# Kernel optimization log

Hardware: AMD Instinct MI355X
Metric: run time of the kernel (lower is better)

The kernel has to match this reference:

```python
import jax, jax.numpy as jnp
import numpy as np

EPS = 1.0
POS_WEIGHT = 1.0
REDUCTION = 'mean'

N, D = 8192, 128
NUM_CLASSES = 32


def setup_inputs() -> dict:
    key = jax.random.key(0)
    k1, k2 = jax.random.split(key)
    ys = jax.random.normal(k1, (N, D), dtype=jnp.float32)
    labels = jax.random.randint(k2, (N,), 0, NUM_CLASSES, dtype=jnp.int64)
    return {"ys": ys, "labels": labels}


def reference(ys, labels):
    n = ys.shape[0]
    # Pairwise squared distances via one GEMM: ||a||^2 + ||b||^2 - 2 a.b
    sq = jnp.sum(ys * ys, axis=-1)                      # [N]
    d2 = sq[:, None] + sq[None, :] - 2.0 * (ys @ ys.T)  # [N, N]
    d2 = jnp.maximum(d2, 0.0)
    pair = jnp.triu(jnp.ones((n, n), dtype=bool), k=1)  # i < j, each unordered pair once
    same = labels[:, None] == labels[None, :]
    # positive-pair term: pos_weight * squared distance
    pos = POS_WEIGHT * d2
    # negative-pair term: clip(eps - sqrt(d2), 0)^2 ; guard sqrt(0) for unused entries
    neg_mask = pair & (~same)
    d = jnp.sqrt(jnp.where(neg_mask, d2, 1.0))
    neg = jnp.clip(EPS - d, 0.0) ** 2
    terms = jnp.where(same, pos, neg) * pair.astype(ys.dtype)
    loss = jnp.sum(terms)
    if REDUCTION == 'mean':
        loss = loss / (n * (n - 1) / 2)
    return loss.reshape(1)
```

## Files before the change

kernel.cpp:

```cpp
#include <hip/hip_runtime.h>
#include <hip/hip_bf16.h>
#include <stdint.h>
#include <math.h>

#define NN 8192
#define DD 128
#define NB 64
#define NBLK (NB * (NB + 1) / 2)

typedef __attribute__((ext_vector_type(8))) short short8;
typedef __attribute__((ext_vector_type(4))) float f32x4;

__device__ __forceinline__ unsigned short f2bf_rne(float x) {
    union { float f; uint32_t u; } v; v.f = x;
    uint32_t r = v.u + 0x7FFFu + ((v.u >> 16) & 1u);
    return (unsigned short)(r >> 16);
}

__global__ __launch_bounds__(256) void prep_kernel(const float* __restrict__ ys,
                                                   unsigned short* __restrict__ ybf,
                                                   float* __restrict__ sq) {
    int row = blockIdx.x * 8 + (threadIdx.x >> 5);
    int c = threadIdx.x & 31;
    float4 v = ((const float4*)(ys + (size_t)row * DD))[c];
    ushort4 o;
    o.x = f2bf_rne(v.x); o.y = f2bf_rne(v.y); o.z = f2bf_rne(v.z); o.w = f2bf_rne(v.w);
    ((ushort4*)(ybf + (size_t)row * DD))[c] = o;
    float s = v.x * v.x + v.y * v.y + v.z * v.z + v.w * v.w;
#pragma unroll
    for (int m = 16; m >= 1; m >>= 1) s += __shfl_xor(s, m);
    if (c == 0) sq[row] = s;
}

__global__ __launch_bounds__(256, 4) void loss_kernel(const unsigned short* __restrict__ ybf,
                                                      const float* __restrict__ sq,
                                                      const int* __restrict__ lab,
                                                      float* __restrict__ partial) {
    int p = blockIdx.x;
    int q = (NBLK - 1) - p;
    int r = (int)((sqrtf(8.0f * (float)q + 1.0f) - 1.0f) * 0.5f);
    while (r * (r + 1) / 2 > q) --r;
    while ((r + 1) * (r + 2) / 2 <= q) ++r;
    int bi = (NB - 1) - r;
    int bj = (NB - 1) - (q - r * (r + 1) / 2);

    __shared__ __align__(16) unsigned char smA[16384];
    __shared__ __align__(16) unsigned char smB[16384];
    __shared__ float sqA[128], sqB[128];
    __shared__ int labA[128], labB[128];
    __shared__ float wsum[4];

    int t = threadIdx.x;
    int i0 = bi * 128, j0 = bj * 128;

    if (t < 128) { sqA[t] = sq[i0 + t]; labA[t] = lab[i0 + t]; }
    else         { int u = t - 128; sqB[u] = sq[j0 + u]; labB[u] = lab[j0 + u]; }

    int wave = t >> 6, lane = t & 63;
    int wm = wave >> 1, wn = wave & 1;
    int lr = lane & 15, lg = lane >> 4;

    f32x4 acc[4][4];
#pragma unroll
    for (int m = 0; m < 4; ++m)
#pragma unroll
        for (int n = 0; n < 4; ++n) acc[m][n] = (f32x4){0.f, 0.f, 0.f, 0.f};

#pragma unroll
    for (int h = 0; h < 2; ++h) {
#pragma unroll
        for (int k = 0; k < 4; ++k) {
            int idx = k * 256 + t;
            int row = idx >> 3, c8 = idx & 7;
            uint4 va = *(const uint4*)(ybf + (size_t)(i0 + row) * DD + h * 64 + c8 * 8);
            uint4 vb = *(const uint4*)(ybf + (size_t)(j0 + row) * DD + h * 64 + c8 * 8);
            *(uint4*)(smA + row * 128 + ((c8 ^ (row & 7)) << 4)) = va;
            *(uint4*)(smB + row * 128 + ((c8 ^ (row & 7)) << 4)) = vb;
        }
        __syncthreads();
#pragma unroll
        for (int ks = 0; ks < 2; ++ks) {
            int c = ks * 4 + lg;
            short8 af[4], bfr[4];
#pragma unroll
            for (int m = 0; m < 4; ++m) {
                int row = wm * 64 + m * 16 + lr;
                af[m] = *(const short8*)(smA + row * 128 + ((c ^ (row & 7)) << 4));
            }
#pragma unroll
            for (int n = 0; n < 4; ++n) {
                int row = wn * 64 + n * 16 + lr;
                bfr[n] = *(const short8*)(smB + row * 128 + ((c ^ (row & 7)) << 4));
            }
#pragma unroll
            for (int m = 0; m < 4; ++m)
#pragma unroll
                for (int n = 0; n < 4; ++n)
                    acc[m][n] = __builtin_amdgcn_mfma_f32_16x16x32_bf16(af[m], bfr[n], acc[m][n], 0, 0, 0);
        }
        __syncthreads();
    }

    float lsum = 0.f;
#pragma unroll
    for (int n = 0; n < 4; ++n) {
        int jl = wn * 64 + n * 16 + lr;
        float sqj = sqB[jl];
        int lj = labB[jl];
        int j = j0 + jl;
#pragma unroll
        for (int m = 0; m < 4; ++m) {
#pragma unroll
            for (int q2 = 0; q2 < 4; ++q2) {
                int il = wm * 64 + m * 16 + lg * 4 + q2;
                int i = i0 + il;
                float d2 = fmaxf(sqA[il] + sqj - 2.0f * acc[m][n][q2], 0.0f);
                float term;
                if (labA[il] == lj) {
                    term = d2;
                } else if (d2 < 1.0f) {
                    float dd = 1.0f - sqrtf(d2);
                    term = dd * dd;
                } else {
                    term = 0.0f;
                }
                if (i < j) lsum += term;
            }
        }
    }

    lsum *= (2.0f / ((float)NN * (float)(NN - 1)));

#pragma unroll
    for (int off = 32; off >= 1; off >>= 1) lsum += __shfl_down(lsum, off);
    if (lane == 0) wsum[wave] = lsum;
    __syncthreads();
    if (t == 0) partial[p] = wsum[0] + wsum[1] + wsum[2] + wsum[3];
}

__global__ __launch_bounds__(256) void reduce_kernel(const float* __restrict__ partial,
                                                     float* __restrict__ out) {
    int t = threadIdx.x;
    float s = 0.f;
    for (int p = t; p < NBLK; p += 256) s += partial[p];
#pragma unroll
    for (int off = 32; off >= 1; off >>= 1) s += __shfl_down(s, off);
    __shared__ float ws[4];
    if ((t & 63) == 0) ws[t >> 6] = s;
    __syncthreads();
    if (t == 0) out[0] = ws[0] + ws[1] + ws[2] + ws[3];
}

extern "C" void kernel_launch(void* const* d_in, const int* in_sizes, int n_in,
                              void* d_out, int out_size, void* d_ws, size_t ws_size,
                              hipStream_t stream) {
    const float* ys = (const float*)d_in[0];
    const int* lab = (const int*)d_in[1];
    float* out = (float*)d_out;

    unsigned short* ybf = (unsigned short*)d_ws;
    float* sq = (float*)((char*)d_ws + (size_t)NN * DD * 2);
    float* partial = (float*)((char*)d_ws + (size_t)NN * DD * 2 + NN * 4);

    prep_kernel<<<NN / 8, 256, 0, stream>>>(ys, ybf, sq);
    loss_kernel<<<NBLK, 256, 0, stream>>>(ybf, sq, lab, partial);
    reduce_kernel<<<1, 256, 0, stream>>>(partial, out);
}
```

Baseline: 34.52 us.

## Compute positive-pair loss via class sums and skip far negative tiles

The positive-pair term now comes in closed form from per-class sums, counts and squared norms (n_c*sum||y||^2 - ||sum y||^2), so the tile loop handles only negative pairs. The ±2 scaling is folded into a negated, rounded bf16 copy of A, and the sq terms are preloaded into the accumulators, so the MFMA output is d2 directly. Operands are stored in an MFMA-fragment layout and read straight from global memory, with no LDS staging or barriers. Wavefronts whose tiles contain no d2 < 1 skip the negative epilogue entirely. In exchange it relies on random data rarely producing close pairs, adds float atomics (making summation order nondeterministic), and the bf16 rounding of the negated copy plus class-sum cancellation may shift accuracy.

```diff
diff --git a/kernel.cpp b/kernel.cpp
--- a/kernel.cpp
+++ b/kernel.cpp
@@ -7,6 +7,8 @@
 #define DD 128
 #define NB 64
 #define NBLK (NB * (NB + 1) / 2)
+#define NC 32
+#define NPB 32
 
 typedef __attribute__((ext_vector_type(8))) short short8;
 typedef __attribute__((ext_vector_type(4))) float f32x4;
@@ -17,138 +19,187 @@
     return (unsigned short)(r >> 16);
 }
 
+
 __global__ __launch_bounds__(256) void prep_kernel(const float* __restrict__ ys,
-                                                   unsigned short* __restrict__ ybf,
-                                                   float* __restrict__ sq) {
-    int row = blockIdx.x * 8 + (threadIdx.x >> 5);
-    int c = threadIdx.x & 31;
-    float4 v = ((const float4*)(ys + (size_t)row * DD))[c];
-    ushort4 o;
-    o.x = f2bf_rne(v.x); o.y = f2bf_rne(v.y); o.z = f2bf_rne(v.z); o.w = f2bf_rne(v.w);
-    ((ushort4*)(ybf + (size_t)row * DD))[c] = o;
-    float s = v.x * v.x + v.y * v.y + v.z * v.z + v.w * v.w;
-#pragma unroll
-    for (int m = 16; m >= 1; m >>= 1) s += __shfl_xor(s, m);
-    if (c == 0) sq[row] = s;
-}
-
-__global__ __launch_bounds__(256, 4) void loss_kernel(const unsigned short* __restrict__ ybf,
-                                                      const float* __restrict__ sq,
-                                                      const int* __restrict__ lab,
-                                                      float* __restrict__ partial) {
-    int p = blockIdx.x;
+                                                   const int* __restrict__ lab,
+                                                   unsigned short* __restrict__ ybfA,
+                                                   unsigned short* __restrict__ ybfB,
+                                                   float* __restrict__ sq,
+                                                   float* __restrict__ clspart,
+                                                   float* __restrict__ clscnt,
+                                                   float* __restrict__ clssq,
+                                                   float* __restrict__ negacc) {
+    int b = blockIdx.x, t = threadIdx.x;
+    __shared__ float cls[NC][DD];
+    __shared__ float cnt[NC], csq[NC];
+    if (b < 512) {
+        int row = b * 16 + (t >> 4), c8 = t & 15;
+        const float* base = ys + (size_t)row * DD + c8 * 8;
+        float4 v0 = *(const float4*)base;
+        float4 v1 = *(const float4*)(base + 4);
+        uint32_t w0 = (uint32_t)f2bf_rne(v0.x) | ((uint32_t)f2bf_rne(v0.y) << 16);
+        uint32_t w1 = (uint32_t)f2bf_rne(v0.z) | ((uint32_t)f2bf_rne(v0.w) << 16);
+        uint32_t w2 = (uint32_t)f2bf_rne(v1.x) | ((uint32_t)f2bf_rne(v1.y) << 16);
+        uint32_t w3 = (uint32_t)f2bf_rne(v1.z) | ((uint32_t)f2bf_rne(v1.w) << 16);
+        uint4 outB = make_uint4(w0, w1, w2, w3);
+        uint4 outA = make_uint4((w0 + 0x00800080u) ^ 0x80008000u,
+                                (w1 + 0x00800080u) ^ 0x80008000u,
+                                (w2 + 0x00800080u) ^ 0x80008000u,
+                                (w3 + 0x00800080u) ^ 0x80008000u);
+        size_t off = (size_t)b * 4096 + c8 * 256 + (row & 15) * 16;
+        *(uint4*)((char*)ybfB + off) = outB;
+        *(uint4*)((char*)ybfA + off) = outA;
+        float s = v0.x * v0.x + v0.y * v0.y + v0.z * v0.z + v0.w * v0.w
+                + v1.x * v1.x + v1.y * v1.y + v1.z * v1.z + v1.w * v1.w;
+        s += __shfl_xor(s, 1); s += __shfl_xor(s, 2);
+        s += __shfl_xor(s, 4); s += __shfl_xor(s, 8);
+        if (c8 == 0) sq[row] = s;
+    } else {
+        int pb = b - 512;
+        for (int i = t; i < NC * DD; i += 256) ((float*)cls)[i] = 0.f;
+        if (t < NC) { cnt[t] = 0.f; csq[t] = 0.f; }
+        __syncthreads();
+        int g = t >> 5, l32 = t & 31;
+        for (int rr = g; rr < 256; rr += 8) {
+            int row = pb * 256 + rr;
+            int lb = lab[row];
+            float4 v = *(const float4*)(ys + (size_t)row * DD + l32 * 4);
+            atomicAdd(&cls[lb][l32 * 4 + 0], v.x);
+            atomicAdd(&cls[lb][l32 * 4 + 1], v.y);
+            atomicAdd(&cls[lb][l32 * 4 + 2], v.z);
+            atomicAdd(&cls[lb][l32 * 4 + 3], v.w);
+            float s = v.x * v.x + v.y * v.y + v.z * v.z + v.w * v.w;
+            s += __shfl_xor(s, 1); s += __shfl_xor(s, 2);
+            s += __shfl_xor(s, 4); s += __shfl_xor(s, 8); s += __shfl_xor(s, 16);
+            if (l32 == 0) { atomicAdd(&cnt[lb], 1.f); atomicAdd(&csq[lb], s); }
+        }
+        __syncthreads();
+        for (int i = t; i < NC * DD; i += 256) clspart[pb * NC * DD + i] = ((float*)cls)[i];
+        if (t < NC) { clscnt[pb * NC + t] = cnt[t]; clssq[pb * NC + t] = csq[t]; }
+        if (pb == 0 && t == 0) *negacc = 0.f;
+    }
+}
+
+__global__ __launch_bounds__(256) void loss_kernel(const unsigned short* __restrict__ ybfA,
+                                                   const unsigned short* __restrict__ ybfB,
+                                                   const float* __restrict__ sq,
+                                                   const int* __restrict__ lab,
+                                                   const float* __restrict__ clspart,
+                                                   const float* __restrict__ clscnt,
+                                                   const float* __restrict__ clssq,
+                                                   float* __restrict__ posval,
+                                                   float* __restrict__ negacc) {
+    int p = blockIdx.x, t = threadIdx.x;
+
+    if (p < NC) {
+        __shared__ float sred[DD];
+        __shared__ float aux[2];
+        if (t < DD) {
+            float S = 0.f;
+            for (int pb = 0; pb < NPB; ++pb) S += clspart[pb * NC * DD + p * DD + t];
+            sred[t] = S * S;
+        } else if (t == 128) {
+            float s = 0.f; for (int pb = 0; pb < NPB; ++pb) s += clscnt[pb * NC + p];
+            aux[0] = s;
+        } else if (t == 129) {
+            float s = 0.f; for (int pb = 0; pb < NPB; ++pb) s += clssq[pb * NC + p];
+            aux[1] = s;
+        }
+        __syncthreads();
+        if (t == 0) {
+            float ssq = 0.f;
+            for (int d = 0; d < DD; ++d) ssq += sred[d];
+            posval[p] = aux[0] * aux[1] - ssq;
+        }
+    }
+
     int q = (NBLK - 1) - p;
     int r = (int)((sqrtf(8.0f * (float)q + 1.0f) - 1.0f) * 0.5f);
     while (r * (r + 1) / 2 > q) --r;
     while ((r + 1) * (r + 2) / 2 <= q) ++r;
     int bi = (NB - 1) - r;
     int bj = (NB - 1) - (q - r * (r + 1) / 2);
-
-    __shared__ __align__(16) unsigned char smA[16384];
-    __shared__ __align__(16) unsigned char smB[16384];
-    __shared__ float sqA[128], sqB[128];
-    __shared__ int labA[128], labB[128];
-    __shared__ float wsum[4];
-
-    int t = threadIdx.x;
     int i0 = bi * 128, j0 = bj * 128;
-
-    if (t < 128) { sqA[t] = sq[i0 + t]; labA[t] = lab[i0 + t]; }
-    else         { int u = t - 128; sqB[u] = sq[j0 + u]; labB[u] = lab[j0 + u]; }
 
     int wave = t >> 6, lane = t & 63;
     int wm = wave >> 1, wn = wave & 1;
     int lr = lane & 15, lg = lane >> 4;
 
+    float sqa[4][4], sqb[4];
+#pragma unroll
+    for (int m = 0; m < 4; ++m)
+#pragma unroll
+        for (int qq = 0; qq < 4; ++qq) sqa[m][qq] = sq[i0 + wm * 64 + m * 16 + lg * 4 + qq];
+#pragma unroll
+    for (int n = 0; n < 4; ++n) sqb[n] = sq[j0 + wn * 64 + n * 16 + lr];
+
     f32x4 acc[4][4];
 #pragma unroll
     for (int m = 0; m < 4; ++m)
 #pragma unroll
-        for (int n = 0; n < 4; ++n) acc[m][n] = (f32x4){0.f, 0.f, 0.f, 0.f};
-
-#pragma unroll
-    for (int h = 0; h < 2; ++h) {
-#pragma unroll
-        for (int k = 0; k < 4; ++k) {
-            int idx = k * 256 + t;
-            int row = idx >> 3, c8 = idx & 7;
-            uint4 va = *(const uint4*)(ybf + (size_t)(i0 + row) * DD + h * 64 + c8 * 8);
-            uint4 vb = *(const uint4*)(ybf + (size_t)(j0 + row) * DD + h * 64 + c8 * 8);
-            *(uint4*)(smA + row * 128 + ((c8 ^ (row & 7)) << 4)) = va;
-            *(uint4*)(smB + row * 128 + ((c8 ^ (row & 7)) << 4)) = vb;
-        }
-        __syncthreads();
-#pragma unroll
-        for (int ks = 0; ks < 2; ++ks) {
-            int c = ks * 4 + lg;
-            short8 af[4], bfr[4];
-#pragma unroll
-            for (int m = 0; m < 4; ++m) {
-                int row = wm * 64 + m * 16 + lr;
-                af[m] = *(const short8*)(smA + row * 128 + ((c ^ (row & 7)) << 4));
-            }
-#pragma unroll
-            for (int n = 0; n < 4; ++n) {
-                int row = wn * 64 + n * 16 + lr;
-                bfr[n] = *(const short8*)(smB + row * 128 + ((c ^ (row & 7)) << 4));
-            }
-#pragma unroll
-            for (int m = 0; m < 4; ++m)
-#pragma unroll
-                for (int n = 0; n < 4; ++n)
-                    acc[m][n] = __builtin_amdgcn_mfma_f32_16x16x32_bf16(af[m], bfr[n], acc[m][n], 0, 0, 0);
-        }
-        __syncthreads();
-    }
-
-    float lsum = 0.f;
-#pragma unroll
-    for (int n = 0; n < 4; ++n) {
-        int jl = wn * 64 + n * 16 + lr;
-        float sqj = sqB[jl];
-        int lj = labB[jl];
-        int j = j0 + jl;
-#pragma unroll
-        for (int m = 0; m < 4; ++m) {
-#pragma unroll
-            for (int q2 = 0; q2 < 4; ++q2) {
-                int il = wm * 64 + m * 16 + lg * 4 + q2;
-                int i = i0 + il;
-                float d2 = fmaxf(sqA[il] + sqj - 2.0f * acc[m][n][q2], 0.0f);
-                float term;
-                if (labA[il] == lj) {
-                    term = d2;
-                } else if (d2 < 1.0f) {
-                    float dd = 1.0f - sqrtf(d2);
-                    term = dd * dd;
-                } else {
-                    term = 0.0f;
+        for (int n = 0; n < 4; ++n) {
+            f32x4 a;
+#pragma unroll
+            for (int qq = 0; qq < 4; ++qq) a[qq] = sqa[m][qq] + sqb[n];
+            acc[m][n] = a;
+        }
+
+    const char* pa = (const char*)ybfA + ((size_t)(i0 >> 4) + wm * 4) * 4096 + lg * 256 + lr * 16;
+    const char* pbp = (const char*)ybfB + ((size_t)(j0 >> 4) + wn * 4) * 4096 + lg * 256 + lr * 16;
+
+#pragma unroll
+    for (int ks = 0; ks < 4; ++ks) {
+        short8 af[4], bf[4];
+#pragma unroll
+        for (int m = 0; m < 4; ++m) af[m] = *(const short8*)(pa + m * 4096 + ks * 1024);
+#pragma unroll
+        for (int n = 0; n < 4; ++n) bf[n] = *(const short8*)(pbp + n * 4096 + ks * 1024);
+#pragma unroll
+        for (int m = 0; m < 4; ++m)
+#pragma unroll
+            for (int n = 0; n < 4; ++n)
+                acc[m][n] = __builtin_amdgcn_mfma_f32_16x16x32_bf16(af[m], bf[n], acc[m][n], 0, 0, 0);
+    }
+
+    float mn = acc[0][0][0];
+#pragma unroll
+    for (int m = 0; m < 4; ++m)
+#pragma unroll
+        for (int n = 0; n < 4; ++n)
+#pragma unroll
+            for (int qq = 0; qq < 4; ++qq) mn = fminf(mn, acc[m][n][qq]);
+
+    if (__any(mn < 1.0f)) {
+        float ns = 0.f;
+#pragma unroll
+        for (int m = 0; m < 4; ++m)
+#pragma unroll
+            for (int n = 0; n < 4; ++n)
+#pragma unroll
+                for (int qq = 0; qq < 4; ++qq) {
+                    float d2 = acc[m][n][qq];
+                    if (d2 < 1.0f) {
+                        int i = i0 + wm * 64 + m * 16 + lg * 4 + qq;
+                        int j = j0 + wn * 64 + n * 16 + lr;
+                        if (i < j && lab[i] != lab[j]) {
+                            float d = sqrtf(fmaxf(d2, 0.f));
+                            float e = 1.0f - d;
+                            ns += e * e;
+                        }
+                    }
                 }
-                if (i < j) lsum += term;
-            }
-        }
-    }
-
-    lsum *= (2.0f / ((float)NN * (float)(NN - 1)));
-
-#pragma unroll
-    for (int off = 32; off >= 1; off >>= 1) lsum += __shfl_down(lsum, off);
-    if (lane == 0) wsum[wave] = lsum;
-    __syncthreads();
-    if (t == 0) partial[p] = wsum[0] + wsum[1] + wsum[2] + wsum[3];
-}
-
-__global__ __launch_bounds__(256) void reduce_kernel(const float* __restrict__ partial,
-                                                     float* __restrict__ out) {
+        if (ns != 0.f) atomicAdd(negacc, ns);
+    }
+}
+
+__global__ __launch_bounds__(64) void finalize_kernel(const float* __restrict__ posval,
+                                                      const float* __restrict__ negacc,
+                                                      float* __restrict__ out) {
     int t = threadIdx.x;
-    float s = 0.f;
-    for (int p = t; p < NBLK; p += 256) s += partial[p];
+    float s = (t < NC) ? posval[t] : 0.f;
 #pragma unroll
     for (int off = 32; off >= 1; off >>= 1) s += __shfl_down(s, off);
-    __shared__ float ws[4];
-    if ((t & 63) == 0) ws[t >> 6] = s;
-    __syncthreads();
-    if (t == 0) out[0] = ws[0] + ws[1] + ws[2] + ws[3];
+    if (t == 0) out[0] = (s + negacc[0]) * (2.0f / ((float)NN * (float)(NN - 1)));
 }
 
 extern "C" void kernel_launch(void* const* d_in, const int* in_sizes, int n_in,
@@ -158,11 +209,17 @@
     const int* lab = (const int*)d_in[1];
     float* out = (float*)d_out;
 
-    unsigned short* ybf = (unsigned short*)d_ws;
-    float* sq = (float*)((char*)d_ws + (size_t)NN * DD * 2);
-    float* partial = (float*)((char*)d_ws + (size_t)NN * DD * 2 + NN * 4);
-
-    prep_kernel<<<NN / 8, 256, 0, stream>>>(ys, ybf, sq);
-    loss_kernel<<<NBLK, 256, 0, stream>>>(ybf, sq, lab, partial);
-    reduce_kernel<<<1, 256, 0, stream>>>(partial, out);
-}
+    char* w = (char*)d_ws;
+    unsigned short* ybfA = (unsigned short*)(w);
+    unsigned short* ybfB = (unsigned short*)(w + 2097152);
+    float* sq      = (float*)(w + 4194304);
+    float* clspart = (float*)(w + 4227072);
+    float* clscnt  = (float*)(w + 4751360);
+    float* clssq   = (float*)(w + 4755456);
+    float* posval  = (float*)(w + 4759552);
+    float* negacc  = (float*)(w + 4759680);
+
+    prep_kernel<<<544, 256, 0, stream>>>(ys, lab, ybfA, ybfB, sq, clspart, clscnt, clssq, negacc);
+    loss_kernel<<<NBLK, 256, 0, stream>>>(ybfA, ybfB, sq, lab, clspart, clscnt, clssq, posval, negacc);
+    finalize_kernel<<<1, 64, 0, stream>>>(posval, negacc, out);
+}
```

Measured after the change: 79.91 us. +131.5%, slower.
